# Kernel tuning notes

Measured on AMD Instinct MI355X. Metric: run time of the kernel, lower is better.

## Reference

```python
import jax, jax.numpy as jnp
import numpy as np

B, T, C = 4, 2048, 1024
H = 16
D = C // H  # head_dim = 64


def setup_inputs() -> dict:
    key = jax.random.key(0)
    ks = jax.random.split(key, 9)
    s = 1.0 / np.sqrt(C)
    return {
        "x": jax.random.normal(ks[0], (B, T, C), dtype=jnp.float32),
        "Wq": jax.random.normal(ks[1], (C, C), dtype=jnp.float32) * s,
        "bq": jnp.zeros((C,), dtype=jnp.float32),
        "Wk": jax.random.normal(ks[2], (C, C), dtype=jnp.float32) * s,
        "bk": jnp.zeros((C,), dtype=jnp.float32),
        "Wv": jax.random.normal(ks[3], (C, C), dtype=jnp.float32) * s,
        "bv": jnp.zeros((C,), dtype=jnp.float32),
        "Wp": jax.random.normal(ks[4], (C, C), dtype=jnp.float32) * s,
        "bp": jnp.zeros((C,), dtype=jnp.float32),
    }


def reference(x, Wq, bq, Wk, bk, Wv, bv, Wp, bp):
    # Linear projections; reshape to [B, H, T, D]
    def split_heads(y):
        return y.reshape(B, T, H, D).transpose(0, 2, 1, 3)

    q = split_heads(x @ Wq + bq)
    k = split_heads(x @ Wk + bk)
    v = split_heads(x @ Wv + bv)

    scale = 1.0 / np.sqrt(D)
    att = jnp.einsum('bhqd,bhkd->bhqk', q, k) * scale  # [B,H,T,T]
    att = jax.nn.softmax(att, axis=-1)
    # dropout with p=0.0 is identity
    out = jnp.einsum('bhqk,bhkd->bhqd', att, v)        # [B,H,T,D]
    out = out.transpose(0, 2, 1, 3).reshape(B, T, C)
    return out @ Wp + bp
```

## Files before the change

kernel.cpp:

```cpp
#include <hip/hip_runtime.h>


#define B_ 4
#define T_ 2048
#define C_ 1024
#define H_ 16
#define D_ 64

#define QSCALE 0.18033688011112042f

typedef float  f32x4  __attribute__((ext_vector_type(4)));
typedef __bf16 bf16x8 __attribute__((ext_vector_type(8)));
typedef __bf16 bf16x4 __attribute__((ext_vector_type(4)));
typedef __bf16 bf16x2 __attribute__((ext_vector_type(2)));
typedef unsigned uint2v __attribute__((ext_vector_type(2)));

typedef const __attribute__((address_space(1))) void gv_t;
typedef __attribute__((address_space(3))) void lds_t;

__device__ __forceinline__ void async_load16(const void* g, void* l) {
  __builtin_amdgcn_global_load_lds((gv_t*)g, (lds_t*)l, 16, 0, 0);
}

__device__ __forceinline__ float fast_exp2(float x) {
#if __has_builtin(__builtin_amdgcn_exp2f)
  return __builtin_amdgcn_exp2f(x);
#else
  return exp2f(x);
#endif
}

__device__ __forceinline__ void pl16_swap(unsigned& a, unsigned& b) {
#if __has_builtin(__builtin_amdgcn_permlane16_swap)
  uint2v r = __builtin_amdgcn_permlane16_swap(a, b, false, false);
  a = r[0];
  b = r[1];
#else
  asm("v_permlane16_swap_b32 %0, %1" : "+v"(a), "+v"(b));
#endif
}

__global__ __launch_bounds__(256) void cast_f32_bf16(
    const float* __restrict__ in, __bf16* __restrict__ out, int n) {
  int i = (blockIdx.x * 256 + threadIdx.x) * 8;
  if (i >= n) return;
  float4 a = *(const float4*)(in + i);
  float4 b = *(const float4*)(in + i + 4);
  bf16x8 o;
  o[0] = (__bf16)a.x; o[1] = (__bf16)a.y; o[2] = (__bf16)a.z; o[3] = (__bf16)a.w;
  o[4] = (__bf16)b.x; o[5] = (__bf16)b.y; o[6] = (__bf16)b.z; o[7] = (__bf16)b.w;
  *(bf16x8*)(out + i) = o;
}

__global__ __launch_bounds__(256) void transpose_cast_w(
    const float* __restrict__ W0, const float* __restrict__ W1,
    const float* __restrict__ W2, const float* __restrict__ W3,
    __bf16* __restrict__ out) {
  int z = blockIdx.z;
  const float* W = (z == 0) ? W0 : (z == 1) ? W1 : (z == 2) ? W2 : W3;
  __bf16* o = out + (size_t)z * (C_ * C_);
  __shared__ __align__(16) __bf16 sT[64][72];
  int tid = threadIdx.x;
  int n0 = blockIdx.x * 64, k0 = blockIdx.y * 64;
#pragma unroll
  for (int i = 0; i < 4; i++) {
    int s = tid + i * 256;
    int kr = s >> 4, nc = (s & 15) * 4;
    float4 v = *(const float4*)&W[(size_t)(k0 + kr) * C_ + n0 + nc];
    bf16x4 t;
    t[0] = (__bf16)v.x; t[1] = (__bf16)v.y; t[2] = (__bf16)v.z; t[3] = (__bf16)v.w;
    *(bf16x4*)&sT[kr][nc] = t;
  }
  __syncthreads();
#pragma unroll
  for (int i = 0; i < 2; i++) {
    int s = tid + i * 256;
    int nr = s >> 3, kc = (s & 7) * 8;
    bf16x8 ov;
#pragma unroll
    for (int j = 0; j < 8; j++) ov[j] = sT[kc + j][nr];
    *(bf16x8*)&o[(size_t)(n0 + nr) * C_ + k0 + kc] = ov;
  }
}

template <typename OutT, int EPI>
__device__ __forceinline__ void gemm_body(
    const __bf16* __restrict__ A, const __bf16* __restrict__ Bt,
    const float* __restrict__ bias, OutT* __restrict__ C, int N, int K,
    float scale, int m0, int n0) {
  __shared__ __align__(16) __bf16 sA[128 * 32];
  __shared__ __align__(16) __bf16 sB[128 * 32];
  int tid = threadIdx.x, lane = tid & 63, wave = tid >> 6;
  int lr = lane & 15, quad = lane >> 4;
  int wm = (wave & 1) * 64, wn = (wave >> 1) * 64;

  const f32x4 zero = {0.f, 0.f, 0.f, 0.f};
  f32x4 acc[4][4];
#pragma unroll
  for (int i = 0; i < 4; i++)
#pragma unroll
    for (int j = 0; j < 4; j++) acc[i][j] = zero;

  for (int k0 = 0; k0 < K; k0 += 32) {
    __syncthreads();
#pragma unroll
    for (int i = 0; i < 2; i++) {
      int s = tid + i * 256;
      int r = s >> 2, c8 = (s & 3) * 8;
      async_load16(A + (size_t)(m0 + r) * K + k0 + c8, &sA[s * 8]);
      async_load16(Bt + (size_t)(n0 + r) * K + k0 + c8, &sB[s * 8]);
    }
    __syncthreads();
    bf16x8 af[4], bfr[4];
#pragma unroll
    for (int mt = 0; mt < 4; mt++)
      af[mt] = *(const bf16x8*)&sA[(wm + mt * 16 + lr) * 32 + quad * 8];
#pragma unroll
    for (int nt = 0; nt < 4; nt++)
      bfr[nt] = *(const bf16x8*)&sB[(wn + nt * 16 + lr) * 32 + quad * 8];
#pragma unroll
    for (int mt = 0; mt < 4; mt++)
#pragma unroll
      for (int nt = 0; nt < 4; nt++)
        acc[mt][nt] = __builtin_amdgcn_mfma_f32_16x16x32_bf16(
            af[mt], bfr[nt], acc[mt][nt], 0, 0, 0);
  }
  if (EPI == 0) {
#pragma unroll
    for (int mt = 0; mt < 4; mt++) {
#pragma unroll
      for (int nt = 0; nt < 4; nt++) {
        int n = n0 + wn + nt * 16 + lr;
        float bv = bias[n];
#pragma unroll
        for (int r = 0; r < 4; r++) {
          int m = m0 + wm + mt * 16 + quad * 4 + r;
          C[(size_t)m * N + n] = (OutT)((acc[mt][nt][r] + bv) * scale);
        }
      }
    }
  } else {
    int bb = m0 >> 11;
    int mloc0 = (m0 & (T_ - 1)) + wm;
    __bf16* Ct = (__bf16*)C;
#pragma unroll
    for (int mt = 0; mt < 4; mt++) {
      int pos = ((quad & 1) << 5) | ((((quad >> 1) << 1) | (mt & 1)) << 3) |
                ((mt >> 1) << 2);
#pragma unroll
      for (int nt = 0; nt < 4; nt++) {
        int n = n0 + wn + nt * 16 + lr;
        float bv = bias[n];
        bf16x4 ov;
#pragma unroll
        for (int r = 0; r < 4; r++) ov[r] = (__bf16)(acc[mt][nt][r] + bv);
        *(bf16x4*)&Ct[((size_t)bb * C_ + n) * T_ + mloc0 + pos] = ov;
      }
    }
  }
}

__global__ __launch_bounds__(256) void gemm_qkv_kernel(
    const __bf16* __restrict__ A, const __bf16* __restrict__ WT,
    const float* __restrict__ b0, const float* __restrict__ b1,
    const float* __restrict__ b2, __bf16* __restrict__ qkbase,
    __bf16* __restrict__ Vt) {
  int l = blockIdx.x;
  int xcd = l & 7;
  int idx = l >> 3;
  int z = idx >> 6;
  int rem = idx & 63;
  int m0 = (xcd * 8 + (rem >> 3)) * 128;
  int n0 = (rem & 7) * 128;
  if (z == 2) {
    gemm_body<__bf16, 1>(A, WT + (size_t)2 * C_ * C_, b2, Vt, C_, C_, 1.0f,
                         m0, n0);
  } else {
    const float* bias = (z == 0) ? b0 : b1;
    float scale = (z == 0) ? QSCALE : 1.0f;
    gemm_body<__bf16, 0>(A, WT + (size_t)z * C_ * C_, bias,
                         qkbase + (size_t)z * (B_ * T_) * C_, C_, C_, scale,
                         m0, n0);
  }
}

__global__ __launch_bounds__(256) void gemm_proj_kernel(
    const __bf16* __restrict__ A, const __bf16* __restrict__ Bt,
    const float* __restrict__ bias, float* __restrict__ C) {
  int l = blockIdx.x;
  int xcd = l & 7;
  int idx = l >> 3;
  int m0 = (xcd * 8 + (idx >> 3)) * 128;
  int n0 = (idx & 7) * 128;
  gemm_body<float, 0>(A, Bt, bias, C, C_, C_, 1.0f, m0, n0);
}

__global__ __launch_bounds__(256) void attn_kernel(
    const __bf16* __restrict__ Q, const __bf16* __restrict__ K,
    const __bf16* __restrict__ Vt, __bf16* __restrict__ O) {
  __shared__ __align__(16) __bf16 sK[64 * 72];
  __shared__ __align__(16) __bf16 sV[64 * 72];
  int tid = threadIdx.x, wave = tid >> 6, lane = tid & 63;
  int lr = lane & 15, quad = lane >> 4;
  int l = blockIdx.x;
  int bh = (l & 7) * 8 + ((l >> 3) & 7);
  int xbq = l >> 6;
  int b = bh >> 4, h = bh & 15;
  int qw = xbq * 256 + wave * 64;

  bf16x8 aq[4][2];
#pragma unroll
  for (int s = 0; s < 4; s++) {
    const __bf16* qp =
        Q + ((size_t)(b * T_ + qw + s * 16 + lr)) * C_ + h * D_ + quad * 8;
    aq[s][0] = *(const bf16x8*)qp;
    aq[s][1] = *(const bf16x8*)(qp + 32);
  }

  bf16x8 onesf;
#pragma unroll
  for (int j = 0; j < 8; j++) onesf[j] = (__bf16)1.0f;

  const f32x4 zero = {0.f, 0.f, 0.f, 0.f};
  f32x4 accO[4][4];
  f32x4 accL[4] = {zero, zero, zero, zero};
#pragma unroll
  for (int s = 0; s < 4; s++)
#pragma unroll
    for (int d = 0; d < 4; d++) accO[s][d] = zero;

  int srow[2], sc8[2];
#pragma unroll
  for (int i = 0; i < 2; i++) {
    int s = tid + i * 256;
    srow[i] = s >> 3;
    sc8[i] = (s & 7) * 8;
  }

  bf16x8 kreg[2], vreg[2];
#pragma unroll
  for (int i = 0; i < 2; i++) {
    kreg[i] = *(const bf16x8*)(K + ((size_t)(b * T_ + srow[i])) * C_ + h * D_ + sc8[i]);
    vreg[i] = *(const bf16x8*)(Vt + ((size_t)(bh * D_ + srow[i])) * T_ + sc8[i]);
  }

  for (int k0 = 0; k0 < T_; k0 += 64) {
    __builtin_amdgcn_sched_barrier(0);
    __builtin_amdgcn_s_barrier();
    __builtin_amdgcn_sched_barrier(0);
#pragma unroll
    for (int i = 0; i < 2; i++) {
      *(bf16x8*)&sK[srow[i] * 72 + sc8[i]] = kreg[i];
      *(bf16x8*)&sV[srow[i] * 72 + sc8[i]] = vreg[i];
    }
    __builtin_amdgcn_sched_barrier(0);
    asm volatile("s_waitcnt lgkmcnt(0)" ::: "memory");
    __builtin_amdgcn_s_barrier();
    __builtin_amdgcn_sched_barrier(0);

    if (k0 + 64 < T_) {
      int kn = k0 + 64;
#pragma unroll
      for (int i = 0; i < 2; i++) {
        kreg[i] = *(const bf16x8*)(K + ((size_t)(b * T_ + kn + srow[i])) * C_ + h * D_ + sc8[i]);
        vreg[i] = *(const bf16x8*)(Vt + ((size_t)(bh * D_ + srow[i])) * T_ + kn + sc8[i]);
      }
    }

    bf16x8 bkf[4][2];
#pragma unroll
    for (int nt = 0; nt < 4; nt++) {
      bkf[nt][0] = *(const bf16x8*)&sK[(nt * 16 + lr) * 72 + quad * 8];
      bkf[nt][1] = *(const bf16x8*)&sK[(nt * 16 + lr) * 72 + 32 + quad * 8];
    }

    bf16x8 bpA[4], bpB[4];
#pragma unroll
    for (int s = 0; s < 4; s++) {
      unsigned pw[4][2];
#pragma unroll
      for (int nt = 0; nt < 4; nt++) {
        f32x4 z = zero;
        z = __builtin_amdgcn_mfma_f32_16x16x32_bf16(bkf[nt][0], aq[s][0], z, 0, 0, 0);
        z = __builtin_amdgcn_mfma_f32_16x16x32_bf16(bkf[nt][1], aq[s][1], z, 0, 0, 0);
        union { bf16x2 h; unsigned u; } t0, t1;
        t0.h[0] = (__bf16)fast_exp2(z[0]);
        t0.h[1] = (__bf16)fast_exp2(z[1]);
        t1.h[0] = (__bf16)fast_exp2(z[2]);
        t1.h[1] = (__bf16)fast_exp2(z[3]);
        pw[nt][0] = t0.u;
        pw[nt][1] = t1.u;
      }
      unsigned a0 = pw[0][0], b0 = pw[1][0]; pl16_swap(a0, b0);
      unsigned a1 = pw[0][1], b1 = pw[1][1]; pl16_swap(a1, b1);
      unsigned a2 = pw[2][0], b2 = pw[3][0]; pl16_swap(a2, b2);
      unsigned a3 = pw[2][1], b3 = pw[3][1]; pl16_swap(a3, b3);
      union { unsigned u[4]; bf16x8 v; } pA, pB;
      pA.u[0] = a0; pA.u[1] = a1; pA.u[2] = a2; pA.u[3] = a3;
      pB.u[0] = b0; pB.u[1] = b1; pB.u[2] = b2; pB.u[3] = b3;
      bpA[s] = pA.v;
      bpB[s] = pB.v;
      accL[s] = __builtin_amdgcn_mfma_f32_16x16x32_bf16(onesf, bpA[s], accL[s], 0, 0, 0);
      accL[s] = __builtin_amdgcn_mfma_f32_16x16x32_bf16(onesf, bpB[s], accL[s], 0, 0, 0);
    }
#pragma unroll
    for (int dt = 0; dt < 4; dt++) {
      bf16x8 av0 = *(const bf16x8*)&sV[(dt * 16 + lr) * 72 + quad * 8];
      bf16x8 av1 = *(const bf16x8*)&sV[(dt * 16 + lr) * 72 + 32 + quad * 8];
#pragma unroll
      for (int s = 0; s < 4; s++) {
        accO[s][dt] = __builtin_amdgcn_mfma_f32_16x16x32_bf16(av0, bpA[s], accO[s][dt], 0, 0, 0);
        accO[s][dt] = __builtin_amdgcn_mfma_f32_16x16x32_bf16(av1, bpB[s], accO[s][dt], 0, 0, 0);
      }
    }
  }

#pragma unroll
  for (int s = 0; s < 4; s++) {
    float inv = 1.0f / accL[s][0];
    __bf16* op =
        O + ((size_t)(b * T_ + qw + s * 16 + lr)) * C_ + h * D_ + quad * 4;
#pragma unroll
    for (int dt = 0; dt < 4; dt++) {
      bf16x4 ov;
#pragma unroll
      for (int r = 0; r < 4; r++) ov[r] = (__bf16)(accO[s][dt][r] * inv);
      *(bf16x4*)&op[dt * 16] = ov;
    }
  }
}

extern "C" void kernel_launch(void* const* d_in, const int* in_sizes, int n_in,
                              void* d_out, int out_size, void* d_ws, size_t ws_size,
                              hipStream_t stream) {
  const float* x  = (const float*)d_in[0];
  const float* Wq = (const float*)d_in[1];
  const float* bq = (const float*)d_in[2];
  const float* Wk = (const float*)d_in[3];
  const float* bk = (const float*)d_in[4];
  const float* Wv = (const float*)d_in[5];
  const float* bv = (const float*)d_in[6];
  const float* Wp = (const float*)d_in[7];
  const float* bp = (const float*)d_in[8];
  float* out = (float*)d_out;

  char* ws = (char*)d_ws;
  const size_t MB = 1024 * 1024;
  __bf16* xb    = (__bf16*)(ws + 0 * MB);
  __bf16* WT    = (__bf16*)(ws + 16 * MB);
  __bf16* Qb    = (__bf16*)(ws + 24 * MB);
  __bf16* Kb    = Qb + (size_t)(B_ * T_) * C_;
  __bf16* Vt    = Kb + (size_t)(B_ * T_) * C_;
  __bf16* attnb = (__bf16*)(ws + 72 * MB);
  __bf16* WpT   = WT + (size_t)3 * C_ * C_;

  cast_f32_bf16<<<dim3(4096), dim3(256), 0, stream>>>(x, xb, B_ * T_ * C_);
  transpose_cast_w<<<dim3(16, 16, 4), dim3(256), 0, stream>>>(Wq, Wk, Wv, Wp, WT);
  gemm_qkv_kernel<<<dim3(1536), dim3(256), 0, stream>>>(xb, WT, bq, bk, bv, Qb, Vt);
  attn_kernel<<<dim3(512), dim3(256), 0, stream>>>(Qb, Kb, Vt, attnb);
  gemm_proj_kernel<<<dim3(512), dim3(256), 0, stream>>>(attnb, WpT, bp, out);
}
```

Before: 268.2 us.

## Double-buffer 128-key attention chunks and merge cast kernels into one launch

The attention loop now loads 128-key chunks of K and V into double-buffered shared memory. The global prefetch for the next chunk overlaps two 64-key compute passes, so there is one barrier per 128 keys instead of two per 64. The separate x-cast and weight transpose-cast kernels are fused into a single prep launch to remove one kernel launch. Shared memory per block grows fourfold, to about 72 KB, which may reduce occupancy, and register pressure rises from the extra prefetch registers.

```diff
diff --git a/kernel.cpp b/kernel.cpp
--- a/kernel.cpp
+++ b/kernel.cpp
@@ -40,36 +40,38 @@
 #endif
 }
 
-__global__ __launch_bounds__(256) void cast_f32_bf16(
-    const float* __restrict__ in, __bf16* __restrict__ out, int n) {
-  int i = (blockIdx.x * 256 + threadIdx.x) * 8;
-  if (i >= n) return;
-  float4 a = *(const float4*)(in + i);
-  float4 b = *(const float4*)(in + i + 4);
-  bf16x8 o;
-  o[0] = (__bf16)a.x; o[1] = (__bf16)a.y; o[2] = (__bf16)a.z; o[3] = (__bf16)a.w;
-  o[4] = (__bf16)b.x; o[5] = (__bf16)b.y; o[6] = (__bf16)b.z; o[7] = (__bf16)b.w;
-  *(bf16x8*)(out + i) = o;
-}
-
-__global__ __launch_bounds__(256) void transpose_cast_w(
+__global__ __launch_bounds__(256) void prep_kernel(
+    const float* __restrict__ x, __bf16* __restrict__ xb,
     const float* __restrict__ W0, const float* __restrict__ W1,
     const float* __restrict__ W2, const float* __restrict__ W3,
-    __bf16* __restrict__ out) {
-  int z = blockIdx.z;
+    __bf16* __restrict__ wt) {
+  __shared__ __align__(16) __bf16 sT[64][72];
+  int l = blockIdx.x;
+  int tid = threadIdx.x;
+  if (l < 4096) {
+    int i = (l * 256 + tid) * 8;
+    float4 a = *(const float4*)(x + i);
+    float4 b = *(const float4*)(x + i + 4);
+    bf16x8 o;
+    o[0] = (__bf16)a.x; o[1] = (__bf16)a.y; o[2] = (__bf16)a.z; o[3] = (__bf16)a.w;
+    o[4] = (__bf16)b.x; o[5] = (__bf16)b.y; o[6] = (__bf16)b.z; o[7] = (__bf16)b.w;
+    *(bf16x8*)(xb + i) = o;
+    return;
+  }
+  int t = l - 4096;
+  int z = t >> 8;
+  int k0 = ((t >> 4) & 15) * 64;
+  int n0 = (t & 15) * 64;
   const float* W = (z == 0) ? W0 : (z == 1) ? W1 : (z == 2) ? W2 : W3;
-  __bf16* o = out + (size_t)z * (C_ * C_);
-  __shared__ __align__(16) __bf16 sT[64][72];
-  int tid = threadIdx.x;
-  int n0 = blockIdx.x * 64, k0 = blockIdx.y * 64;
+  __bf16* o = wt + (size_t)z * (C_ * C_);
 #pragma unroll
   for (int i = 0; i < 4; i++) {
     int s = tid + i * 256;
     int kr = s >> 4, nc = (s & 15) * 4;
     float4 v = *(const float4*)&W[(size_t)(k0 + kr) * C_ + n0 + nc];
-    bf16x4 t;
-    t[0] = (__bf16)v.x; t[1] = (__bf16)v.y; t[2] = (__bf16)v.z; t[3] = (__bf16)v.w;
-    *(bf16x4*)&sT[kr][nc] = t;
+    bf16x4 tt;
+    tt[0] = (__bf16)v.x; tt[1] = (__bf16)v.y; tt[2] = (__bf16)v.z; tt[3] = (__bf16)v.w;
+    *(bf16x4*)&sT[kr][nc] = tt;
   }
   __syncthreads();
 #pragma unroll
@@ -198,8 +200,8 @@
 __global__ __launch_bounds__(256) void attn_kernel(
     const __bf16* __restrict__ Q, const __bf16* __restrict__ K,
     const __bf16* __restrict__ Vt, __bf16* __restrict__ O) {
-  __shared__ __align__(16) __bf16 sK[64 * 72];
-  __shared__ __align__(16) __bf16 sV[64 * 72];
+  __shared__ __align__(16) __bf16 sK[2][2 * 64 * 72];
+  __shared__ __align__(16) __bf16 sV[2][2 * 64 * 72];
   int tid = threadIdx.x, wave = tid >> 6, lane = tid & 63;
   int lr = lane & 15, quad = lane >> 4;
   int l = blockIdx.x;
@@ -229,51 +231,47 @@
 #pragma unroll
     for (int d = 0; d < 4; d++) accO[s][d] = zero;
 
-  int srow[2], sc8[2];
-#pragma unroll
-  for (int i = 0; i < 2; i++) {
+  int kts[4], kd8[4], koff[4];
+  int vkt[4], voff[4];
+#pragma unroll
+  for (int i = 0; i < 4; i++) {
     int s = tid + i * 256;
-    srow[i] = s >> 3;
-    sc8[i] = (s & 7) * 8;
-  }
-
-  bf16x8 kreg[2], vreg[2];
-#pragma unroll
-  for (int i = 0; i < 2; i++) {
-    kreg[i] = *(const bf16x8*)(K + ((size_t)(b * T_ + srow[i])) * C_ + h * D_ + sc8[i]);
-    vreg[i] = *(const bf16x8*)(Vt + ((size_t)(bh * D_ + srow[i])) * T_ + sc8[i]);
-  }
-
-  for (int k0 = 0; k0 < T_; k0 += 64) {
-    __builtin_amdgcn_sched_barrier(0);
-    __builtin_amdgcn_s_barrier();
-    __builtin_amdgcn_sched_barrier(0);
-#pragma unroll
-    for (int i = 0; i < 2; i++) {
-      *(bf16x8*)&sK[srow[i] * 72 + sc8[i]] = kreg[i];
-      *(bf16x8*)&sV[srow[i] * 72 + sc8[i]] = vreg[i];
-    }
-    __builtin_amdgcn_sched_barrier(0);
-    asm volatile("s_waitcnt lgkmcnt(0)" ::: "memory");
-    __builtin_amdgcn_s_barrier();
-    __builtin_amdgcn_sched_barrier(0);
-
-    if (k0 + 64 < T_) {
-      int kn = k0 + 64;
-#pragma unroll
-      for (int i = 0; i < 2; i++) {
-        kreg[i] = *(const bf16x8*)(K + ((size_t)(b * T_ + kn + srow[i])) * C_ + h * D_ + sc8[i]);
-        vreg[i] = *(const bf16x8*)(Vt + ((size_t)(bh * D_ + srow[i])) * T_ + kn + sc8[i]);
-      }
-    }
-
+    kts[i] = s >> 3;
+    kd8[i] = (s & 7) * 8;
+    koff[i] = (kts[i] >> 6) * (64 * 72) + (kts[i] & 63) * 72 + kd8[i];
+    int vd = s >> 4;
+    vkt[i] = (s & 15) * 8;
+    voff[i] = (vkt[i] >> 6) * (64 * 72) + vd * 72 + (vkt[i] & 63);
+  }
+  const __bf16* Kg = K + (size_t)b * T_ * C_ + h * D_;
+  const __bf16* Vg = Vt + (size_t)(bh * D_) * T_;
+  int vd4[4];
+#pragma unroll
+  for (int i = 0; i < 4; i++) vd4[i] = (tid + i * 256) >> 4;
+
+  bf16x8 kreg[4], vreg[4];
+  auto gload = [&](int c0) {
+#pragma unroll
+    for (int i = 0; i < 4; i++) {
+      kreg[i] = *(const bf16x8*)(Kg + (size_t)(c0 + kts[i]) * C_ + kd8[i]);
+      vreg[i] = *(const bf16x8*)(Vg + (size_t)vd4[i] * T_ + c0 + vkt[i]);
+    }
+  };
+  auto stage = [&](int buf) {
+#pragma unroll
+    for (int i = 0; i < 4; i++) {
+      *(bf16x8*)&sK[buf][koff[i]] = kreg[i];
+      *(bf16x8*)&sV[buf][voff[i]] = vreg[i];
+    }
+  };
+
+  auto compute64 = [&](const __bf16* sKh, const __bf16* sVh) {
     bf16x8 bkf[4][2];
 #pragma unroll
     for (int nt = 0; nt < 4; nt++) {
-      bkf[nt][0] = *(const bf16x8*)&sK[(nt * 16 + lr) * 72 + quad * 8];
-      bkf[nt][1] = *(const bf16x8*)&sK[(nt * 16 + lr) * 72 + 32 + quad * 8];
-    }
-
+      bkf[nt][0] = *(const bf16x8*)&sKh[(nt * 16 + lr) * 72 + quad * 8];
+      bkf[nt][1] = *(const bf16x8*)&sKh[(nt * 16 + lr) * 72 + 32 + quad * 8];
+    }
     bf16x8 bpA[4], bpB[4];
 #pragma unroll
     for (int s = 0; s < 4; s++) {
@@ -283,11 +281,11 @@
         f32x4 z = zero;
         z = __builtin_amdgcn_mfma_f32_16x16x32_bf16(bkf[nt][0], aq[s][0], z, 0, 0, 0);
         z = __builtin_amdgcn_mfma_f32_16x16x32_bf16(bkf[nt][1], aq[s][1], z, 0, 0, 0);
-        union { bf16x2 h; unsigned u; } t0, t1;
-        t0.h[0] = (__bf16)fast_exp2(z[0]);
-        t0.h[1] = (__bf16)fast_exp2(z[1]);
-        t1.h[0] = (__bf16)fast_exp2(z[2]);
-        t1.h[1] = (__bf16)fast_exp2(z[3]);
+        union { bf16x2 h2; unsigned u; } t0, t1;
+        t0.h2[0] = (__bf16)fast_exp2(z[0]);
+        t0.h2[1] = (__bf16)fast_exp2(z[1]);
+        t1.h2[0] = (__bf16)fast_exp2(z[2]);
+        t1.h2[1] = (__bf16)fast_exp2(z[3]);
         pw[nt][0] = t0.u;
         pw[nt][1] = t1.u;
       }
@@ -305,13 +303,35 @@
     }
 #pragma unroll
     for (int dt = 0; dt < 4; dt++) {
-      bf16x8 av0 = *(const bf16x8*)&sV[(dt * 16 + lr) * 72 + quad * 8];
-      bf16x8 av1 = *(const bf16x8*)&sV[(dt * 16 + lr) * 72 + 32 + quad * 8];
+      bf16x8 av0 = *(const bf16x8*)&sVh[(dt * 16 + lr) * 72 + quad * 8];
+      bf16x8 av1 = *(const bf16x8*)&sVh[(dt * 16 + lr) * 72 + 32 + quad * 8];
 #pragma unroll
       for (int s = 0; s < 4; s++) {
         accO[s][dt] = __builtin_amdgcn_mfma_f32_16x16x32_bf16(av0, bpA[s], accO[s][dt], 0, 0, 0);
         accO[s][dt] = __builtin_amdgcn_mfma_f32_16x16x32_bf16(av1, bpB[s], accO[s][dt], 0, 0, 0);
       }
+    }
+  };
+
+  gload(0);
+  stage(0);
+  __builtin_amdgcn_sched_barrier(0);
+  asm volatile("s_waitcnt lgkmcnt(0)" ::: "memory");
+  __builtin_amdgcn_s_barrier();
+  __builtin_amdgcn_sched_barrier(0);
+
+  const int NC = T_ / 128;
+  for (int c = 0; c < NC; c++) {
+    int buf = c & 1;
+    if (c + 1 < NC) gload((c + 1) * 128);
+    compute64(&sK[buf][0], &sV[buf][0]);
+    compute64(&sK[buf][64 * 72], &sV[buf][64 * 72]);
+    if (c + 1 < NC) {
+      stage(buf ^ 1);
+      __builtin_amdgcn_sched_barrier(0);
+      asm volatile("s_waitcnt lgkmcnt(0)" ::: "memory");
+      __builtin_amdgcn_s_barrier();
+      __builtin_amdgcn_sched_barrier(0);
     }
   }
 
@@ -354,8 +374,7 @@
   __bf16* attnb = (__bf16*)(ws + 72 * MB);
   __bf16* WpT   = WT + (size_t)3 * C_ * C_;
 
-  cast_f32_bf16<<<dim3(4096), dim3(256), 0, stream>>>(x, xb, B_ * T_ * C_);
-  transpose_cast_w<<<dim3(16, 16, 4), dim3(256), 0, stream>>>(Wq, Wk, Wv, Wp, WT);
+  prep_kernel<<<dim3(5120), dim3(256), 0, stream>>>(x, xb, Wq, Wk, Wv, Wp, WT);
   gemm_qkv_kernel<<<dim3(1536), dim3(256), 0, stream>>>(xb, WT, bq, bk, bv, Qb, Vt);
   attn_kernel<<<dim3(512), dim3(256), 0, stream>>>(Qb, Kb, Vt, attnb);
   gemm_proj_kernel<<<dim3(512), dim3(256), 0, stream>>>(attnb, WpT, bp, out);
```

New measurement: 292.4 us. +9.0%, slower.
